# Performance work log

Measured on AMD Instinct MI355X. Metric: run time of the kernel, lower is better.

Reference implementation:

```python
import jax, jax.numpy as jnp
import numpy as np

D = 512
N_WAY = 64
K_SHOT = 16
N_QUERY = 8192


def setup_inputs() -> dict:
    key = jax.random.key(0)
    k1, k2, k3, k4 = jax.random.split(key, 4)
    support = jax.random.normal(k1, (N_WAY * K_SHOT, D), dtype=jnp.float32)
    query = jax.random.normal(k2, (N_QUERY, D), dtype=jnp.float32)
    # nn.Linear(input_dim, input_dim) params (kaiming-uniform-ish scale)
    bound = 1.0 / np.sqrt(D)
    W = jax.random.uniform(k3, (D, D), minval=-bound, maxval=bound, dtype=jnp.float32)
    b = jax.random.uniform(k4, (D,), minval=-bound, maxval=bound, dtype=jnp.float32)
    return {"support": support, "query": query, "W": W, "b": b,
            "n_way": N_WAY, "k_shot": K_SHOT}


def reference(support, query, W, b, n_way, k_shot):
    # shared linear projection: x @ W^T + b (torch nn.Linear convention)
    support_emb = support @ W.T + b            # [n_way*k_shot, d]
    query_emb = query @ W.T + b                # [n_q, d]
    # class prototypes: mean over the k_shot axis
    prototypes = support_emb.reshape(n_way, k_shot, -1).mean(axis=1)  # [n_way, d]
    # pairwise squared euclidean distances (broadcast sub/square/sum,
    # same math as the torch euclidean_dist)
    diff = query_emb[:, None, :] - prototypes[None, :, :]  # [n_q, n_way, d]
    dists = jnp.sum(diff * diff, axis=-1)                  # [n_q, n_way]
    return dists
```

## Files before the change

kernel.cpp:

```cpp
#include <hip/hip_runtime.h>
#include <hip/hip_bf16.h>

#define D 512
#define NWAY 64
#define KSHOT 16
#define NQ 8192

typedef __bf16 bf16_t;
typedef __bf16 bf16x8_t __attribute__((ext_vector_type(8)));
typedef float  f32x4    __attribute__((ext_vector_type(4)));

typedef __attribute__((address_space(1))) const void gv_t;
typedef __attribute__((address_space(3))) void lv_t;
__device__ __forceinline__ void ld16(const void* g, void* l) {
    __builtin_amdgcn_global_load_lds((gv_t*)g, (lv_t*)l, 16, 0, 0);
}


__global__ __launch_bounds__(256) void k_prep1(
    const float* __restrict__ sup, const float* __restrict__ W,
    const float* __restrict__ bias, float* __restrict__ Pg,
    bf16_t* __restrict__ Bsw)
{
    const int b = blockIdx.x, t = threadIdx.x;

    if (b < 256) {
        const int c = b >> 2, jq = b & 3;
        __shared__ __align__(16) float cm[D];
        {
            const int d = t * 2;
            float sx = 0.f, sy = 0.f;
#pragma unroll
            for (int j = 0; j < KSHOT; ++j) {
                float2 v = *(const float2*)(sup + (size_t)(c * KSHOT + j) * D + d);
                sx += v.x; sy += v.y;
            }
            cm[d] = sx * (1.0f / KSHOT); cm[d + 1] = sy * (1.0f / KSHOT);
        }
        __syncthreads();
        const int j = jq * 128 + (t >> 1);
        const int half = t & 1;
        const f32x4* wr = (const f32x4*)(W + (size_t)j * D + half * 256);
        const f32x4* cr = (const f32x4*)(cm + half * 256);
        float s = 0.f;
#pragma unroll 8
        for (int i = 0; i < 64; ++i) {
            f32x4 a = cr[i], wv = wr[i];
            s += a[0]*wv[0] + a[1]*wv[1] + a[2]*wv[2] + a[3]*wv[3];
        }
        s += __shfl_xor(s, 1);
        if (!half) Pg[(size_t)c * D + j] = s + bias[j];
        return;
    }

    {
        const int n = (b - 256) * 4 + (t >> 6);
        const int sl = t & 63;
        const f32x4* wp = (const f32x4*)(W + (size_t)n * D + sl * 8);
        f32x4 v0 = wp[0], v1 = wp[1];
        bf16x8_t hv = { (bf16_t)v0[0], (bf16_t)v0[1], (bf16_t)v0[2], (bf16_t)v0[3],
                        (bf16_t)v1[0], (bf16_t)v1[1], (bf16_t)v1[2], (bf16_t)v1[3] };
        const int ck = sl >> 3, s = sl & 7;
        *(bf16x8_t*)(Bsw + (size_t)ck * 36864 + n * 64 + ((s ^ (n & 7)) * 8)) = hv;
    }
}

__global__ __launch_bounds__(256) void k_prep2(
    const float* __restrict__ Pg, const float* __restrict__ W,
    const float* __restrict__ bias, bf16_t* __restrict__ Bsw,
    float* __restrict__ ph)
{
    __shared__ __align__(16) float Pl[D];
    __shared__ float sG[2][128];
    __shared__ float red[4];

    const int c = blockIdx.x >> 2, kc = blockIdx.x & 3;
    const int t = threadIdx.x;
    const int kl = t & 127, jh = t >> 7;
    const int k = kc * 128 + kl;

    ((float2*)Pl)[t] = ((const float2*)(Pg + (size_t)c * D))[t];
    __syncthreads();

    float g = 0.f;
    const float* wcol = W + (size_t)jh * 256 * D + k;
#pragma unroll 8
    for (int j = 0; j < 256; ++j)
        g += Pl[jh * 256 + j] * wcol[(size_t)j * D];
    sG[jh][kl] = g;

    if (kc == 0) {
        float v1 = Pl[t], v2 = Pl[t + 256];
        float pp = v1 * v1 - 2.0f * bias[t] * v1 + v2 * v2 - 2.0f * bias[t + 256] * v2;
#pragma unroll
        for (int off = 32; off; off >>= 1) pp += __shfl_xor(pp, off);
        if ((t & 63) == 0) red[t >> 6] = pp;
    }
    __syncthreads();

    if (jh == 0) {
        const float gt = sG[0][kl] + sG[1][kl];
        const int n = 512 + c;
        const int ck = k >> 6, s = (k >> 3) & 7, e = k & 7;
        Bsw[(size_t)ck * 36864 + n * 64 + ((s ^ (c & 7)) * 8) + e] = (bf16_t)gt;
    }
    if (kc == 0 && t == 0) ph[c] = red[0] + red[1] + red[2] + red[3];
}

__global__ __launch_bounds__(512, 2) void k_main(
    const float* __restrict__ query, const bf16_t* __restrict__ Bsw,
    const float* __restrict__ bias, const float* __restrict__ ph,
    float* __restrict__ out)
{
    __shared__ bf16_t Bb[36864];
    __shared__ bf16_t Ab[2048];
    __shared__ float qln[4][32];
    __shared__ float phs[NWAY];
    __shared__ float bs[576];

    const int t = threadIdx.x, bm = blockIdx.x;
    bs[t < 512 ? t : 511] = bias[t < 512 ? t : 511];
    if (t < NWAY) { bs[512 + t] = 0.f; phs[t] = ph[t]; }

    const int l = t & 63, w = t >> 6;
    const int wm = w & 1, wn = w >> 1;
    const int r15 = l & 15, quad = l >> 4;

    const int xt0 = ((quad ^ (r15 & 7)) * 8);
    const int xt1 = (((4 + quad) ^ (r15 & 7)) * 8);
    const int aoff = (wm * 16 + r15) * 64;
    const int boff = (wn * 144 + r15) * 64;

    const int am = (w * 64 + l) >> 3;
    const int as = l & 7;
    const float* aq = query + (size_t)(bm * 32 + am) * D + as * 8;
    bf16_t* adst = Ab + am * 64 + ((as ^ (am & 7)) * 8);

    f32x4 acc[9];
#pragma unroll
    for (int i = 0; i < 9; ++i) acc[i] = (f32x4){0.f, 0.f, 0.f, 0.f};

    for (int ck = 0; ck < 8; ++ck) {
        if (ck) __syncthreads();
        if (w < 4) {
            f32x4 v0 = *(const f32x4*)(aq + ck * 64);
            f32x4 v1 = *(const f32x4*)(aq + ck * 64 + 4);
            bf16x8_t hv = { (bf16_t)v0[0], (bf16_t)v0[1], (bf16_t)v0[2], (bf16_t)v0[3],
                            (bf16_t)v1[0], (bf16_t)v1[1], (bf16_t)v1[2], (bf16_t)v1[3] };
            *(bf16x8_t*)adst = hv;
        }
        {
            const int wb = w * 4608 + l * 8;
#pragma unroll
            for (int i = 0; i < 9; ++i) {
                const int off = wb + i * 512;
                ld16(Bsw + (size_t)ck * 36864 + off, Bb + off);
            }
        }
        __syncthreads();

        bf16x8_t a0 = *(const bf16x8_t*)(Ab + aoff + xt0);
        bf16x8_t a1 = *(const bf16x8_t*)(Ab + aoff + xt1);
#pragma unroll
        for (int tt = 0; tt < 9; ++tt) {
            bf16x8_t b0 = *(const bf16x8_t*)(Bb + boff + tt * 1024 + xt0);
            bf16x8_t b1 = *(const bf16x8_t*)(Bb + boff + tt * 1024 + xt1);
            acc[tt] = __builtin_amdgcn_mfma_f32_16x16x32_bf16(a0, b0, acc[tt], 0, 0, 0);
            acc[tt] = __builtin_amdgcn_mfma_f32_16x16x32_bf16(a1, b1, acc[tt], 0, 0, 0);
        }
    }

    float qp[4] = {0.f, 0.f, 0.f, 0.f};
#pragma unroll
    for (int tt = 0; tt < 9; ++tt) {
        const int colbase = wn * 144 + tt * 16;
        const float m = (colbase < 512) ? 1.f : 0.f;
        const float bv = bs[colbase + r15];
#pragma unroll
        for (int reg = 0; reg < 4; ++reg) {
            float v = acc[tt][reg] + bv;
            qp[reg] += m * v * v;
        }
    }
#pragma unroll
    for (int reg = 0; reg < 4; ++reg) {
        float s = qp[reg];
        s += __shfl_xor(s, 1); s += __shfl_xor(s, 2);
        s += __shfl_xor(s, 4); s += __shfl_xor(s, 8);
        if (r15 == 0) qln[wn][wm * 16 + quad * 4 + reg] = s;
    }
    __syncthreads();

    if (wn == 3) {
#pragma unroll
        for (int reg = 0; reg < 4; ++reg) {
            const int row_local = quad * 4 + reg;
            const float qt = qln[0][wm * 16 + row_local] + qln[1][wm * 16 + row_local] +
                             qln[2][wm * 16 + row_local] + qln[3][wm * 16 + row_local];
            const int rowg = bm * 32 + wm * 16 + row_local;
#pragma unroll
            for (int tg = 0; tg < 4; ++tg) {
                const int c = tg * 16 + r15;
                out[(size_t)rowg * NWAY + c] = qt + phs[c] - 2.0f * acc[5 + tg][reg];
            }
        }
    }
}

extern "C" void kernel_launch(void* const* d_in, const int* in_sizes, int n_in,
                              void* d_out, int out_size, void* d_ws, size_t ws_size,
                              hipStream_t stream)
{
    const float* support = (const float*)d_in[0];
    const float* query   = (const float*)d_in[1];
    const float* W       = (const float*)d_in[2];
    const float* bias    = (const float*)d_in[3];
    float* out = (float*)d_out;

    char* ws = (char*)d_ws;
    bf16_t* Bsw = (bf16_t*)ws;
    float*  ph  = (float*)(ws + 589824);
    float*  Pg  = (float*)(ws + 589824 + 256);

    k_prep1<<<384, 256, 0, stream>>>(support, W, bias, Pg, Bsw);
    k_prep2<<<256, 256, 0, stream>>>(Pg, W, bias, Bsw, ph);
    k_main<<<256, 512, 0, stream>>>(query, Bsw, bias, ph, out);
}
```

Measured before the change: 110.8 us.

## Merge prep kernels with atomic counter handoff and prefetch query chunks in main

Fuses the two prep kernels into one 640-block launch. The prototype-consumer blocks spin on per-class atomic counters, released by the producer blocks, instead of waiting at a kernel boundary. The main GEMM loop now issues global loads of the next query chunk into registers before the current compute, hiding load latency. This adds a memset launch and a spin-wait that depends on producer blocks being scheduled before or alongside the waiting blocks, which could deadlock or stall if blocks are not co-resident.

```diff
diff --git a/kernel.cpp b/kernel.cpp
--- a/kernel.cpp
+++ b/kernel.cpp
@@ -17,10 +17,10 @@
 }
 
 
-__global__ __launch_bounds__(256) void k_prep1(
+__global__ __launch_bounds__(256) void k_prep(
     const float* __restrict__ sup, const float* __restrict__ W,
     const float* __restrict__ bias, float* __restrict__ Pg,
-    bf16_t* __restrict__ Bsw)
+    bf16_t* __restrict__ Bsw, float* __restrict__ ph, int* __restrict__ cnt)
 {
     const int b = blockIdx.x, t = threadIdx.x;
 
@@ -50,10 +50,14 @@
         }
         s += __shfl_xor(s, 1);
         if (!half) Pg[(size_t)c * D + j] = s + bias[j];
+        __threadfence();
+        __syncthreads();
+        if (t == 0)
+            __hip_atomic_fetch_add(&cnt[c], 1, __ATOMIC_RELEASE, __HIP_MEMORY_SCOPE_AGENT);
         return;
     }
 
-    {
+    if (b < 384) {
         const int n = (b - 256) * 4 + (t >> 6);
         const int sl = t & 63;
         const f32x4* wp = (const f32x4*)(W + (size_t)n * D + sl * 8);
@@ -62,20 +66,17 @@
                         (bf16_t)v1[0], (bf16_t)v1[1], (bf16_t)v1[2], (bf16_t)v1[3] };
         const int ck = sl >> 3, s = sl & 7;
         *(bf16x8_t*)(Bsw + (size_t)ck * 36864 + n * 64 + ((s ^ (n & 7)) * 8)) = hv;
-    }
-}
-
-__global__ __launch_bounds__(256) void k_prep2(
-    const float* __restrict__ Pg, const float* __restrict__ W,
-    const float* __restrict__ bias, bf16_t* __restrict__ Bsw,
-    float* __restrict__ ph)
-{
+        return;
+    }
+
+    const int c = (b - 384) >> 2, kc = (b - 384) & 3;
     __shared__ __align__(16) float Pl[D];
     __shared__ float sG[2][128];
     __shared__ float red[4];
 
-    const int c = blockIdx.x >> 2, kc = blockIdx.x & 3;
-    const int t = threadIdx.x;
+    while (__hip_atomic_load(&cnt[c], __ATOMIC_ACQUIRE, __HIP_MEMORY_SCOPE_AGENT) < 4)
+        __builtin_amdgcn_s_sleep(8);
+
     const int kl = t & 127, jh = t >> 7;
     const int k = kc * 128 + kl;
 
@@ -101,8 +102,8 @@
     if (jh == 0) {
         const float gt = sG[0][kl] + sG[1][kl];
         const int n = 512 + c;
-        const int ck = k >> 6, s = (k >> 3) & 7, e = k & 7;
-        Bsw[(size_t)ck * 36864 + n * 64 + ((s ^ (c & 7)) * 8) + e] = (bf16_t)gt;
+        const int ckk = k >> 6, s = (k >> 3) & 7, e = k & 7;
+        Bsw[(size_t)ckk * 36864 + n * 64 + ((s ^ (c & 7)) * 8) + e] = (bf16_t)gt;
     }
     if (kc == 0 && t == 0) ph[c] = red[0] + red[1] + red[2] + red[3];
 }
@@ -119,7 +120,7 @@
     __shared__ float bs[576];
 
     const int t = threadIdx.x, bm = blockIdx.x;
-    bs[t < 512 ? t : 511] = bias[t < 512 ? t : 511];
+    if (t < 512) bs[t] = bias[t];
     if (t < NWAY) { bs[512 + t] = 0.f; phs[t] = ph[t]; }
 
     const int l = t & 63, w = t >> 6;
@@ -140,15 +141,11 @@
 #pragma unroll
     for (int i = 0; i < 9; ++i) acc[i] = (f32x4){0.f, 0.f, 0.f, 0.f};
 
+    f32x4 a0, a1;
+    if (w < 4) { a0 = *(const f32x4*)(aq); a1 = *(const f32x4*)(aq + 4); }
+
     for (int ck = 0; ck < 8; ++ck) {
         if (ck) __syncthreads();
-        if (w < 4) {
-            f32x4 v0 = *(const f32x4*)(aq + ck * 64);
-            f32x4 v1 = *(const f32x4*)(aq + ck * 64 + 4);
-            bf16x8_t hv = { (bf16_t)v0[0], (bf16_t)v0[1], (bf16_t)v0[2], (bf16_t)v0[3],
-                            (bf16_t)v1[0], (bf16_t)v1[1], (bf16_t)v1[2], (bf16_t)v1[3] };
-            *(bf16x8_t*)adst = hv;
-        }
         {
             const int wb = w * 4608 + l * 8;
 #pragma unroll
@@ -157,16 +154,25 @@
                 ld16(Bsw + (size_t)ck * 36864 + off, Bb + off);
             }
         }
+        if (w < 4) {
+            bf16x8_t hv = { (bf16_t)a0[0], (bf16_t)a0[1], (bf16_t)a0[2], (bf16_t)a0[3],
+                            (bf16_t)a1[0], (bf16_t)a1[1], (bf16_t)a1[2], (bf16_t)a1[3] };
+            *(bf16x8_t*)adst = hv;
+        }
         __syncthreads();
-
-        bf16x8_t a0 = *(const bf16x8_t*)(Ab + aoff + xt0);
-        bf16x8_t a1 = *(const bf16x8_t*)(Ab + aoff + xt1);
+        if (w < 4 && ck < 7) {
+            a0 = *(const f32x4*)(aq + (ck + 1) * 64);
+            a1 = *(const f32x4*)(aq + (ck + 1) * 64 + 4);
+        }
+
+        bf16x8_t fa0 = *(const bf16x8_t*)(Ab + aoff + xt0);
+        bf16x8_t fa1 = *(const bf16x8_t*)(Ab + aoff + xt1);
 #pragma unroll
         for (int tt = 0; tt < 9; ++tt) {
             bf16x8_t b0 = *(const bf16x8_t*)(Bb + boff + tt * 1024 + xt0);
             bf16x8_t b1 = *(const bf16x8_t*)(Bb + boff + tt * 1024 + xt1);
-            acc[tt] = __builtin_amdgcn_mfma_f32_16x16x32_bf16(a0, b0, acc[tt], 0, 0, 0);
-            acc[tt] = __builtin_amdgcn_mfma_f32_16x16x32_bf16(a1, b1, acc[tt], 0, 0, 0);
+            acc[tt] = __builtin_amdgcn_mfma_f32_16x16x32_bf16(fa0, b0, acc[tt], 0, 0, 0);
+            acc[tt] = __builtin_amdgcn_mfma_f32_16x16x32_bf16(fa1, b1, acc[tt], 0, 0, 0);
         }
     }
 
@@ -221,8 +227,9 @@
     bf16_t* Bsw = (bf16_t*)ws;
     float*  ph  = (float*)(ws + 589824);
     float*  Pg  = (float*)(ws + 589824 + 256);
-
-    k_prep1<<<384, 256, 0, stream>>>(support, W, bias, Pg, Bsw);
-    k_prep2<<<256, 256, 0, stream>>>(Pg, W, bias, Bsw, ph);
+    int*    cnt = (int*)(ws + 589824 + 256 + 131072);
+
+    hipMemsetAsync(cnt, 0, NWAY * sizeof(int), stream);
+    k_prep<<<640, 256, 0, stream>>>(support, W, bias, Pg, Bsw, ph, cnt);
     k_main<<<256, 512, 0, stream>>>(query, Bsw, bias, ph, out);
 }
```

After: 222.2 us. 2x slower.

## Halve K-chunk to 32 to fit four blocks per CU and prefetch query

Applied to the files above, without the earlier changes.

The K chunk per LDS stage shrinks from 64 to 32, so the B tile buffer is halved and the weight swizzle is rewritten for a 4-way XOR pattern. This lets launch bounds request four resident blocks per CU. The loop now runs 16 iterations, and the next query chunk is loaded into registers during the current chunk's MFMAs. The shared bias copy is replaced by direct global reads in the epilogue. The price is twice as many barriers and fewer MFMAs between them, plus tighter register limits.

```diff
diff --git a/kernel.cpp b/kernel.cpp
--- a/kernel.cpp
+++ b/kernel.cpp
@@ -60,8 +60,8 @@
         f32x4 v0 = wp[0], v1 = wp[1];
         bf16x8_t hv = { (bf16_t)v0[0], (bf16_t)v0[1], (bf16_t)v0[2], (bf16_t)v0[3],
                         (bf16_t)v1[0], (bf16_t)v1[1], (bf16_t)v1[2], (bf16_t)v1[3] };
-        const int ck = sl >> 3, s = sl & 7;
-        *(bf16x8_t*)(Bsw + (size_t)ck * 36864 + n * 64 + ((s ^ (n & 7)) * 8)) = hv;
+        const int ck = sl >> 2, s = sl & 3;
+        *(bf16x8_t*)(Bsw + (size_t)ck * 18432 + n * 32 + ((s ^ (n & 3)) * 8)) = hv;
     }
 }
 
@@ -101,72 +101,74 @@
     if (jh == 0) {
         const float gt = sG[0][kl] + sG[1][kl];
         const int n = 512 + c;
-        const int ck = k >> 6, s = (k >> 3) & 7, e = k & 7;
-        Bsw[(size_t)ck * 36864 + n * 64 + ((s ^ (c & 7)) * 8) + e] = (bf16_t)gt;
+        const int ck = k >> 5, s = (k >> 3) & 3, e = k & 7;
+        Bsw[(size_t)ck * 18432 + n * 32 + ((s ^ (c & 3)) * 8) + e] = (bf16_t)gt;
     }
     if (kc == 0 && t == 0) ph[c] = red[0] + red[1] + red[2] + red[3];
 }
 
-__global__ __launch_bounds__(512, 2) void k_main(
+__global__ __launch_bounds__(512, 4) void k_main(
     const float* __restrict__ query, const bf16_t* __restrict__ Bsw,
     const float* __restrict__ bias, const float* __restrict__ ph,
     float* __restrict__ out)
 {
-    __shared__ bf16_t Bb[36864];
-    __shared__ bf16_t Ab[2048];
+    __shared__ bf16_t Bb[18432];
+    __shared__ bf16_t Ab[1024];
     __shared__ float qln[4][32];
     __shared__ float phs[NWAY];
-    __shared__ float bs[576];
 
     const int t = threadIdx.x, bm = blockIdx.x;
-    bs[t < 512 ? t : 511] = bias[t < 512 ? t : 511];
-    if (t < NWAY) { bs[512 + t] = 0.f; phs[t] = ph[t]; }
+    if (t < NWAY) phs[t] = ph[t];
 
     const int l = t & 63, w = t >> 6;
     const int wm = w & 1, wn = w >> 1;
     const int r15 = l & 15, quad = l >> 4;
 
-    const int xt0 = ((quad ^ (r15 & 7)) * 8);
-    const int xt1 = (((4 + quad) ^ (r15 & 7)) * 8);
-    const int aoff = (wm * 16 + r15) * 64;
-    const int boff = (wn * 144 + r15) * 64;
-
-    const int am = (w * 64 + l) >> 3;
-    const int as = l & 7;
-    const float* aq = query + (size_t)(bm * 32 + am) * D + as * 8;
-    bf16_t* adst = Ab + am * 64 + ((as ^ (am & 7)) * 8);
+    const int xt   = ((quad ^ (r15 & 3)) * 8);
+    const int aoff = (wm * 16 + r15) * 32 + xt;
+    const int boff = (wn * 144 + r15) * 32;
+
+    const int am = t >> 2, as = t & 3;
+    const float* aq = query + (size_t)(bm * 32 + (am & 31)) * D + as * 8;
+    const int adst = (am & 31) * 32 + ((as ^ (am & 3)) * 8);
 
     f32x4 acc[9];
 #pragma unroll
     for (int i = 0; i < 9; ++i) acc[i] = (f32x4){0.f, 0.f, 0.f, 0.f};
 
-    for (int ck = 0; ck < 8; ++ck) {
+    f32x4 a0, a1;
+    if (t < 128) { a0 = *(const f32x4*)(aq); a1 = *(const f32x4*)(aq + 4); }
+
+    for (int ck = 0; ck < 16; ++ck) {
         if (ck) __syncthreads();
-        if (w < 4) {
-            f32x4 v0 = *(const f32x4*)(aq + ck * 64);
-            f32x4 v1 = *(const f32x4*)(aq + ck * 64 + 4);
-            bf16x8_t hv = { (bf16_t)v0[0], (bf16_t)v0[1], (bf16_t)v0[2], (bf16_t)v0[3],
-                            (bf16_t)v1[0], (bf16_t)v1[1], (bf16_t)v1[2], (bf16_t)v1[3] };
-            *(bf16x8_t*)adst = hv;
+        if (t < 128) {
+            bf16x8_t hv = { (bf16_t)a0[0], (bf16_t)a0[1], (bf16_t)a0[2], (bf16_t)a0[3],
+                            (bf16_t)a1[0], (bf16_t)a1[1], (bf16_t)a1[2], (bf16_t)a1[3] };
+            *(bf16x8_t*)(Ab + adst) = hv;
         }
         {
-            const int wb = w * 4608 + l * 8;
-#pragma unroll
-            for (int i = 0; i < 9; ++i) {
-                const int off = wb + i * 512;
-                ld16(Bsw + (size_t)ck * 36864 + off, Bb + off);
+            const bf16_t* src = Bsw + (size_t)ck * 18432;
+#pragma unroll
+            for (int i = 0; i < 4; ++i) {
+                const int off = (w * 4 + i) * 512 + l * 8;
+                ld16(src + off, Bb + off);
+            }
+            if (w < 4) {
+                const int off = (32 + w) * 512 + l * 8;
+                ld16(src + off, Bb + off);
             }
         }
         __syncthreads();
-
-        bf16x8_t a0 = *(const bf16x8_t*)(Ab + aoff + xt0);
-        bf16x8_t a1 = *(const bf16x8_t*)(Ab + aoff + xt1);
+        if (t < 128 && ck < 15) {
+            a0 = *(const f32x4*)(aq + (ck + 1) * 32);
+            a1 = *(const f32x4*)(aq + (ck + 1) * 32 + 4);
+        }
+
+        bf16x8_t fa = *(const bf16x8_t*)(Ab + aoff);
 #pragma unroll
         for (int tt = 0; tt < 9; ++tt) {
-            bf16x8_t b0 = *(const bf16x8_t*)(Bb + boff + tt * 1024 + xt0);
-            bf16x8_t b1 = *(const bf16x8_t*)(Bb + boff + tt * 1024 + xt1);
-            acc[tt] = __builtin_amdgcn_mfma_f32_16x16x32_bf16(a0, b0, acc[tt], 0, 0, 0);
-            acc[tt] = __builtin_amdgcn_mfma_f32_16x16x32_bf16(a1, b1, acc[tt], 0, 0, 0);
+            bf16x8_t fb = *(const bf16x8_t*)(Bb + boff + tt * 512 + xt);
+            acc[tt] = __builtin_amdgcn_mfma_f32_16x16x32_bf16(fa, fb, acc[tt], 0, 0, 0);
         }
     }
 
@@ -175,7 +177,8 @@
     for (int tt = 0; tt < 9; ++tt) {
         const int colbase = wn * 144 + tt * 16;
         const float m = (colbase < 512) ? 1.f : 0.f;
-        const float bv = bs[colbase + r15];
+        const int bi = colbase + r15;
+        const float bv = bias[bi < 512 ? bi : 511];
 #pragma unroll
         for (int reg = 0; reg < 4; ++reg) {
             float v = acc[tt][reg] + bv;
```

Result: slower. 115.9 us (+4.5%).
